# Performance work log

Measured on AMD Instinct MI355X. Metric: run time of the kernel, lower is better.

Reference implementation:

```python
import jax, jax.numpy as jnp
import numpy as np

SEQ, D, H = 4096, 1024, 16
HD = D // H
SCALE = HD ** -0.5


def setup_inputs() -> dict:
    key = jax.random.key(0)
    ks = jax.random.split(key, 8)
    s = 0.02
    return {
        "hidden_states": jax.random.normal(ks[0], (SEQ, D), dtype=jnp.float32),
        "wq": jax.random.normal(ks[1], (D, D), dtype=jnp.float32) * s,
        "bq": jax.random.normal(ks[2], (D,), dtype=jnp.float32) * s,
        "wk": jax.random.normal(ks[3], (D, D), dtype=jnp.float32) * s,
        "wv": jax.random.normal(ks[4], (D, D), dtype=jnp.float32) * s,
        "bv": jax.random.normal(ks[5], (D,), dtype=jnp.float32) * s,
        "wo": jax.random.normal(ks[6], (D, D), dtype=jnp.float32) * s,
        "bo": jax.random.normal(ks[7], (D,), dtype=jnp.float32) * s,
    }


def reference(hidden_states, wq, bq, wk, wv, bv, wo, bo):
    S = hidden_states.shape[0]
    # torch Linear: y = x @ W^T + b  (k_proj has no bias)
    q = (hidden_states @ wq.T + bq).reshape(S, H, HD).transpose(1, 0, 2)  # [H,S,hd]
    k = (hidden_states @ wk.T).reshape(S, H, HD).transpose(1, 0, 2)       # [H,S,hd]
    v = (hidden_states @ wv.T + bv).reshape(S, H, HD).transpose(1, 0, 2)  # [H,S,hd]
    scores = jnp.einsum('hqd,hkd->hqk', q, k) * SCALE                     # [H,S,S]
    # softmax computed in fp32 then cast back to query dtype
    attn = jax.nn.softmax(scores.astype(jnp.float32), axis=-1).astype(q.dtype)
    out = jnp.einsum('hqk,hkd->hqd', attn, v)                             # [H,S,hd]
    out = out.transpose(1, 0, 2).reshape(S, D)
    return out @ wo.T + bo
```

## Files before the change

kernel.cpp:

```cpp
#include <hip/hip_runtime.h>

#define SEQ 4096
#define DIM 1024
#define NH 16
#define HD 64
#define QKVSTR 3072

typedef __attribute__((ext_vector_type(8))) short bf16x8;
typedef __attribute__((ext_vector_type(4))) float f32x4;
typedef __attribute__((ext_vector_type(16))) float f32x16;
typedef __attribute__((ext_vector_type(4))) unsigned int uint4v;

__device__ __forceinline__ unsigned short f2bf(float f) {
  unsigned int b = __float_as_uint(f);
  b = b + 0x7fffu + ((b >> 16) & 1u);
  return (unsigned short)(b >> 16);
}

__device__ __forceinline__ unsigned int cvt_pk_bf16(float lo, float hi) {
  unsigned int r;
  asm("v_cvt_pk_bf16_f32 %0, %1, %2" : "=v"(r) : "v"(lo), "v"(hi));
  return r;
}

__device__ __forceinline__ float fast_exp2(float x) {
#if __has_builtin(__builtin_amdgcn_exp2f)
  return __builtin_amdgcn_exp2f(x);
#else
  float r; asm("v_exp_f32 %0, %1" : "=v"(r) : "v"(x)); return r;
#endif
}

typedef __attribute__((address_space(3))) unsigned int lds_uint;
typedef __attribute__((address_space(1))) const unsigned int global_uint;

__device__ __forceinline__ void gload_lds16(const void* g, void* l) {
  __builtin_amdgcn_global_load_lds((global_uint*)g, (lds_uint*)l, 16, 0, 0);
}

__global__ __launch_bounds__(256) void cast_all_kernel(
    const float* __restrict__ X, const float* __restrict__ wq, const float* __restrict__ wk,
    const float* __restrict__ wv, const float* __restrict__ wo,
    unsigned short* __restrict__ Xb, unsigned short* __restrict__ Wqkv,
    unsigned short* __restrict__ Wob, float qscale) {
  int i = blockIdx.x * 256 + threadIdx.x;
  const float* src;
  unsigned short* dst;
  float sc = 1.f;
  if (i < 524288) { src = X + (size_t)i * 8; dst = Xb + (size_t)i * 8; }
  else if (i < 655360) { int j = i - 524288; src = wq + (size_t)j * 8; dst = Wqkv + (size_t)j * 8; sc = qscale; }
  else if (i < 786432) { int j = i - 655360; src = wk + (size_t)j * 8; dst = Wqkv + 1048576 + (size_t)j * 8; }
  else if (i < 917504) { int j = i - 786432; src = wv + (size_t)j * 8; dst = Wqkv + 2097152 + (size_t)j * 8; }
  else { int j = i - 917504; src = wo + (size_t)j * 8; dst = Wob + (size_t)j * 8; }
  const float4* p = (const float4*)src;
  float4 x0 = p[0], x1 = p[1];
  union { unsigned short u[8]; uint4v v; } o;
  o.u[0] = f2bf(x0.x * sc); o.u[1] = f2bf(x0.y * sc);
  o.u[2] = f2bf(x0.z * sc); o.u[3] = f2bf(x0.w * sc);
  o.u[4] = f2bf(x1.x * sc); o.u[5] = f2bf(x1.y * sc);
  o.u[6] = f2bf(x1.z * sc); o.u[7] = f2bf(x1.w * sc);
  *(uint4v*)dst = o.v;
}

template<int BIASMODE, int OUT_F32>
__global__ __launch_bounds__(256) void gemm_bt_kernel(
    const unsigned short* __restrict__ A, const unsigned short* __restrict__ B,
    const float* __restrict__ b0, const float* __restrict__ b1, float qscale,
    void* __restrict__ Cout, int M, int N, int K) {
  __shared__ unsigned short As[2][128 * 32];
  __shared__ unsigned short Bs[2][128 * 32];
  int tid = threadIdx.x;
  int wave = tid >> 6, lane = tid & 63;
  int g = lane >> 4, lc = lane & 15;
  int wm = wave >> 1, wn = wave & 1;

  int gx = gridDim.x;
  int wgid = blockIdx.y * gx + blockIdx.x;
  int cpx = (gx * gridDim.y) >> 3;
  int sw = (wgid & 7) * cpx + (wgid >> 3);
  int m0 = (sw / gx) * 128, n0 = (sw % gx) * 128;

  int ch0 = wave * 64 + lane;
  int r0 = ch0 >> 2, cb0 = ch0 & 3;
  int ch1 = 256 + ch0;
  int r1 = ch1 >> 2, cb1 = ch1 & 3;
  const unsigned short* Ar0 = A + (size_t)(m0 + r0) * K + cb0 * 8;
  const unsigned short* Ar1 = A + (size_t)(m0 + r1) * K + cb1 * 8;
  const unsigned short* Br0 = B + (size_t)(n0 + r0) * K + cb0 * 8;
  const unsigned short* Br1 = B + (size_t)(n0 + r1) * K + cb1 * 8;
  unsigned short* sAlo[2] = { &As[0][(wave * 64) * 8],       &As[1][(wave * 64) * 8] };
  unsigned short* sAhi[2] = { &As[0][(256 + wave * 64) * 8], &As[1][(256 + wave * 64) * 8] };
  unsigned short* sBlo[2] = { &Bs[0][(wave * 64) * 8],       &Bs[1][(wave * 64) * 8] };
  unsigned short* sBhi[2] = { &Bs[0][(256 + wave * 64) * 8], &Bs[1][(256 + wave * 64) * 8] };

  f32x4 acc[4][4] = {};

  gload_lds16(Ar0, sAlo[0]);
  gload_lds16(Ar1, sAhi[0]);
  gload_lds16(Br0, sBlo[0]);
  gload_lds16(Br1, sBhi[0]);

  int cur = 0;
  for (int k0 = 0; k0 < K; k0 += 32) {
    {
      int kn = (k0 + 32 < K) ? (k0 + 32) : 0;
      int nb = cur ^ 1;
      gload_lds16(Ar0 + kn, sAlo[nb]);
      gload_lds16(Ar1 + kn, sAhi[nb]);
      gload_lds16(Br0 + kn, sBlo[nb]);
      gload_lds16(Br1 + kn, sBhi[nb]);
    }
    asm volatile("s_waitcnt vmcnt(4)" ::: "memory");
    __builtin_amdgcn_sched_barrier(0);
    __builtin_amdgcn_s_barrier();
    __builtin_amdgcn_sched_barrier(0);

    bf16x8 af[4], bfr[4];
    for (int mf = 0; mf < 4; ++mf)
      af[mf] = *(const bf16x8*)&As[cur][(wm * 64 + mf * 16 + lc) * 32 + g * 8];
    for (int nf = 0; nf < 4; ++nf)
      bfr[nf] = *(const bf16x8*)&Bs[cur][(wn * 64 + nf * 16 + lc) * 32 + g * 8];
    for (int mf = 0; mf < 4; ++mf)
      for (int nf = 0; nf < 4; ++nf)
        acc[mf][nf] = __builtin_amdgcn_mfma_f32_16x16x32_bf16(af[mf], bfr[nf], acc[mf][nf], 0, 0, 0);

    asm volatile("" ::: "memory");
    __builtin_amdgcn_sched_barrier(0);
    __builtin_amdgcn_s_barrier();
    cur ^= 1;
  }

  for (int nf = 0; nf < 4; ++nf) {
    int col = n0 + wn * 64 + nf * 16 + lc;
    float bias = 0.f;
    if (BIASMODE == 1) {
      int sect = col >> 10, cc = col & 1023;
      bias = (sect == 0) ? b0[cc] * qscale : ((sect == 2) ? b1[cc] : 0.f);
    } else if (BIASMODE == 2) {
      bias = b0[col];
    }
    for (int mf = 0; mf < 4; ++mf) {
      int row = m0 + wm * 64 + mf * 16 + g * 4;
      for (int r = 0; r < 4; ++r) {
        float v = acc[mf][nf][r] + bias;
        if (OUT_F32) ((float*)Cout)[(size_t)(row + r) * N + col] = v;
        else ((unsigned short*)Cout)[(size_t)(row + r) * N + col] = f2bf(v);
      }
    }
  }
}

__global__ __launch_bounds__(256) void transpose_kernel(
    const unsigned short* __restrict__ V, unsigned short* __restrict__ Vt) {
  __shared__ unsigned short Ts[64 * 72];
  int tid = threadIdx.x;
  int s0 = blockIdx.x * 64, d0 = blockIdx.y * 64;
  for (int c = 0; c < 2; ++c) {
    int q = c * 256 + tid;
    int r = q >> 3, cb = q & 7;
    uint4v v = *(const uint4v*)&V[(size_t)(s0 + r) * QKVSTR + d0 + cb * 8];
    *(uint4v*)&Ts[r * 72 + cb * 8] = v;
  }
  __syncthreads();
  for (int c = 0; c < 2; ++c) {
    int q = c * 256 + tid;
    int d = q >> 3, sc = q & 7;
    union { unsigned short u[8]; uint4v v; } ov;
    for (int j = 0; j < 8; ++j) ov.u[j] = Ts[(sc * 8 + j) * 72 + d];
    *(uint4v*)&Vt[(size_t)(d0 + d) * SEQ + s0 + sc * 8] = ov.v;
  }
}

__global__ __launch_bounds__(256) void attn_kernel(
    const unsigned short* __restrict__ QKV, const unsigned short* __restrict__ Vt,
    unsigned short* __restrict__ Aout) {
  __shared__ unsigned short Qs[128 * 64];
  __shared__ unsigned short Ks[2][64 * 64];
  __shared__ unsigned short Vs[2][64 * 64];
  int tid = threadIdx.x;
  int w = tid >> 6, lane = tid & 63;
  int hi = lane >> 5, l31 = lane & 31;

  int bid = blockIdx.x;
  int swz = (bid & 7) * 64 + (bid >> 3);
  int h = swz >> 5;
  int q0 = (swz & 31) * 128;

  const unsigned short* Qg = QKV + h * HD;
  const unsigned short* Kg = QKV + DIM + h * HD;
  const unsigned short* Vg = Vt + (size_t)(h * HD) * SEQ;

  int ch0 = w * 64 + lane;
  int r0s = ch0 >> 3, d0s = (ch0 & 7) ^ (r0s & 7);
  int ch1 = 256 + ch0;
  int r1s = ch1 >> 3, d1s = (ch1 & 7) ^ (r1s & 7);
  size_t koff0 = (size_t)r0s * QKVSTR + d0s * 8;
  size_t koff1 = (size_t)r1s * QKVSTR + d1s * 8;
  size_t voff0 = (size_t)r0s * SEQ + d0s * 8;
  size_t voff1 = (size_t)r1s * SEQ + d1s * 8;
  unsigned short* ldsK_lo[2] = { &Ks[0][(w * 64) * 8],       &Ks[1][(w * 64) * 8] };
  unsigned short* ldsK_hi[2] = { &Ks[0][(256 + w * 64) * 8], &Ks[1][(256 + w * 64) * 8] };
  unsigned short* ldsV_lo[2] = { &Vs[0][(w * 64) * 8],       &Vs[1][(w * 64) * 8] };
  unsigned short* ldsV_hi[2] = { &Vs[0][(256 + w * 64) * 8], &Vs[1][(256 + w * 64) * 8] };

  for (int c = 0; c < 4; ++c) {
    int chunk = c * 256 + w * 64 + lane;
    int row = chunk >> 3, pos = chunk & 7;
    int db = pos ^ (row & 7);
    gload_lds16(Qg + (size_t)(q0 + row) * QKVSTR + db * 8, Qs + (c * 256 + w * 64) * 8);
  }
  gload_lds16(Kg + koff0, ldsK_lo[0]);
  gload_lds16(Kg + koff1, ldsK_hi[0]);
  gload_lds16(Vg + voff0, ldsV_lo[0]);
  gload_lds16(Vg + voff1, ldsV_hi[0]);
  asm volatile("s_waitcnt vmcnt(4)" ::: "memory");
  __builtin_amdgcn_sched_barrier(0);
  __builtin_amdgcn_s_barrier();

  bf16x8 qf[4];
  {
    int qrow = w * 32 + l31;
    for (int dc = 0; dc < 4; ++dc) {
      int pos = 2 * dc + hi;
      qf[dc] = *(const bf16x8*)&Qs[qrow * 64 + (pos ^ (qrow & 7)) * 8];
    }
  }

  int offb[4];
#pragma unroll
  for (int dc = 0; dc < 4; ++dc)
    offb[dc] = l31 * 128 + (((2 * dc + hi) ^ (l31 & 7)) * 16);
  const char* KbA = (const char*)&Ks[0][0];
  const char* KbB = (const char*)&Ks[1][0];
  const char* VbA = (const char*)&Vs[0][0];
  const char* VbB = (const char*)&Vs[1][0];

  union { unsigned short us[8]; bf16x8 v; } one8;
#pragma unroll
  for (int j = 0; j < 8; ++j) one8.us[j] = 0x3F80;

  f32x16 o0 = {}, o1 = {}, lsa = {};
  int cur = 0;

  for (int t = 0; t < SEQ / 64; ++t) {
    {
      int kvn = ((t + 1) & (SEQ / 64 - 1)) * 64;
      const unsigned short* Kt = Kg + (size_t)kvn * QKVSTR;
      const unsigned short* Vtt = Vg + kvn;
      int nb = cur ^ 1;
      gload_lds16(Kt + koff0, ldsK_lo[nb]);
      gload_lds16(Kt + koff1, ldsK_hi[nb]);
      gload_lds16(Vtt + voff0, ldsV_lo[nb]);
      gload_lds16(Vtt + voff1, ldsV_hi[nb]);
    }
    asm volatile("s_waitcnt vmcnt(4)" ::: "memory");
    __builtin_amdgcn_sched_barrier(0);
    __builtin_amdgcn_s_barrier();
    __builtin_amdgcn_sched_barrier(0);

    const char* Kb = cur ? KbB : KbA;
    const char* Vb = cur ? VbB : VbA;

    bf16x8 kf0[4], kf1[4];
#pragma unroll
    for (int dc = 0; dc < 4; ++dc) {
      kf0[dc] = *(const bf16x8*)(Kb + offb[dc]);
      kf1[dc] = *(const bf16x8*)(Kb + offb[dc] + 4096);
    }
    f32x16 st0 = {}, st1 = {};
    __builtin_amdgcn_s_setprio(1);
#pragma unroll
    for (int dc = 0; dc < 4; ++dc) {
      st0 = __builtin_amdgcn_mfma_f32_32x32x16_bf16(kf0[dc], qf[dc], st0, 0, 0, 0);
      st1 = __builtin_amdgcn_mfma_f32_32x32x16_bf16(kf1[dc], qf[dc], st1, 0, 0, 0);
    }
    __builtin_amdgcn_s_setprio(0);

    bf16x8 vf0[4], vf1[4];
#pragma unroll
    for (int c = 0; c < 4; ++c) {
      vf0[c] = *(const bf16x8*)(Vb + offb[c]);
      vf1[c] = *(const bf16x8*)(Vb + offb[c] + 4096);
    }

    float p0[16], p1[16];
#pragma unroll
    for (int r = 0; r < 16; ++r) p0[r] = fast_exp2(st0[r]);
#pragma unroll
    for (int r = 0; r < 16; ++r) p1[r] = fast_exp2(st1[r]);

    bf16x8 pa[4];
#pragma unroll
    for (int f = 0; f < 2; ++f) {
      const float* pp = f ? p1 : p0;
#pragma unroll
      for (int cc = 0; cc < 2; ++cc) {
        unsigned uLO0 = cvt_pk_bf16(pp[8 * cc + 0], pp[8 * cc + 1]);
        unsigned uLO1 = cvt_pk_bf16(pp[8 * cc + 2], pp[8 * cc + 3]);
        unsigned uHI0 = cvt_pk_bf16(pp[8 * cc + 4], pp[8 * cc + 5]);
        unsigned uHI1 = cvt_pk_bf16(pp[8 * cc + 6], pp[8 * cc + 7]);
        auto s0 = __builtin_amdgcn_permlane32_swap(uLO0, uHI0, false, false);
        auto s1 = __builtin_amdgcn_permlane32_swap(uLO1, uHI1, false, false);
        union { unsigned u[4]; bf16x8 v; } pw;
        pw.u[0] = s0[0]; pw.u[1] = s1[0]; pw.u[2] = s0[1]; pw.u[3] = s1[1];
        pa[f * 2 + cc] = pw.v;
      }
    }

    __builtin_amdgcn_s_setprio(1);
#pragma unroll
    for (int c = 0; c < 4; ++c) {
      o0 = __builtin_amdgcn_mfma_f32_32x32x16_bf16(pa[c], vf0[c], o0, 0, 0, 0);
      o1 = __builtin_amdgcn_mfma_f32_32x32x16_bf16(pa[c], vf1[c], o1, 0, 0, 0);
      lsa = __builtin_amdgcn_mfma_f32_32x32x16_bf16(pa[c], one8.v, lsa, 0, 0, 0);
    }
    __builtin_amdgcn_s_setprio(0);

    asm volatile("" ::: "memory");
    __builtin_amdgcn_sched_barrier(0);
    __builtin_amdgcn_s_barrier();
    cur ^= 1;
  }

  float* Qf = (float*)Qs;
  if (l31 == 0) {
#pragma unroll
    for (int r = 0; r < 16; ++r)
      Qf[w * 32 + ((r & 3) + 8 * (r >> 2) + 4 * hi)] = lsa[r];
  }
  float inv = 1.f / Qf[w * 32 + l31];
#pragma unroll
  for (int r = 0; r < 16; ++r) {
    int qr = (r & 3) + 8 * (r >> 2) + 4 * hi;
    float ir = __shfl(inv, qr + (lane & 32));
    size_t row = q0 + w * 32 + qr;
    Aout[row * DIM + h * HD + l31]      = f2bf(o0[r] * ir);
    Aout[row * DIM + h * HD + 32 + l31] = f2bf(o1[r] * ir);
  }
}

extern "C" void kernel_launch(void* const* d_in, const int* in_sizes, int n_in,
                              void* d_out, int out_size, void* d_ws, size_t ws_size,
                              hipStream_t stream) {
  (void)in_sizes; (void)n_in; (void)out_size; (void)ws_size;
  const float* X  = (const float*)d_in[0];
  const float* wq = (const float*)d_in[1];
  const float* bq = (const float*)d_in[2];
  const float* wk = (const float*)d_in[3];
  const float* wv = (const float*)d_in[4];
  const float* bv = (const float*)d_in[5];
  const float* wo = (const float*)d_in[6];
  const float* bo = (const float*)d_in[7];

  char* ws = (char*)d_ws;
  const size_t SZ_XD  = (size_t)SEQ * DIM * 2;
  const size_t SZ_W   = (size_t)DIM * DIM * 2;
  const size_t SZ_QKV = (size_t)SEQ * QKVSTR * 2;
  unsigned short* Xb   = (unsigned short*)(ws);
  unsigned short* Wqkv = (unsigned short*)(ws + SZ_XD);
  unsigned short* Wob  = (unsigned short*)(ws + SZ_XD + 3 * SZ_W);
  unsigned short* QKVb = (unsigned short*)(ws + SZ_XD + 4 * SZ_W);
  unsigned short* Vtb  = (unsigned short*)(ws + SZ_XD + 4 * SZ_W + SZ_QKV);
  unsigned short* Ab   = Xb;

  const float QSCALE = 0.125f * 1.44269504088896f;

  cast_all_kernel<<<4096, 256, 0, stream>>>(X, wq, wk, wv, wo, Xb, Wqkv, Wob, QSCALE);

  gemm_bt_kernel<1, 0><<<dim3(QKVSTR / 128, SEQ / 128), 256, 0, stream>>>(
      Xb, Wqkv, bq, bv, QSCALE, QKVb, SEQ, QKVSTR, DIM);

  transpose_kernel<<<dim3(SEQ / 64, DIM / 64), 256, 0, stream>>>(QKVb + 2 * DIM, Vtb);

  attn_kernel<<<SEQ / 128 * NH, 256, 0, stream>>>(QKVb, Vtb, Ab);

  gemm_bt_kernel<2, 1><<<dim3(DIM / 128, SEQ / 128), 256, 0, stream>>>(
      Ab, Wob, bo, nullptr, 1.f, d_out, SEQ, DIM, DIM);
}
```

Measured before the change: 167.3 us.

## Process two 64-key tiles per barrier with 128-key double-buffered LDS stages

The attention main loop now loads 128 keys/values per stage into a doubled LDS buffer and runs the 64-key compute body twice per iteration. This halves the number of block-wide barriers and wait points, and deepens each prefetch. In exchange LDS use roughly doubles (Q plus 4x K/V tiles), which can lower occupancy, and the unrolled body doubles the code size.

```diff
diff --git a/kernel.cpp b/kernel.cpp
--- a/kernel.cpp
+++ b/kernel.cpp
@@ -175,8 +175,8 @@
     const unsigned short* __restrict__ QKV, const unsigned short* __restrict__ Vt,
     unsigned short* __restrict__ Aout) {
   __shared__ unsigned short Qs[128 * 64];
-  __shared__ unsigned short Ks[2][64 * 64];
-  __shared__ unsigned short Vs[2][64 * 64];
+  __shared__ unsigned short Ks[2][2][64 * 64];
+  __shared__ unsigned short Vs[2][2][64 * 64];
   int tid = threadIdx.x;
   int w = tid >> 6, lane = tid & 63;
   int hi = lane >> 5, l31 = lane & 31;
@@ -198,10 +198,16 @@
   size_t koff1 = (size_t)r1s * QKVSTR + d1s * 8;
   size_t voff0 = (size_t)r0s * SEQ + d0s * 8;
   size_t voff1 = (size_t)r1s * SEQ + d1s * 8;
-  unsigned short* ldsK_lo[2] = { &Ks[0][(w * 64) * 8],       &Ks[1][(w * 64) * 8] };
-  unsigned short* ldsK_hi[2] = { &Ks[0][(256 + w * 64) * 8], &Ks[1][(256 + w * 64) * 8] };
-  unsigned short* ldsV_lo[2] = { &Vs[0][(w * 64) * 8],       &Vs[1][(w * 64) * 8] };
-  unsigned short* ldsV_hi[2] = { &Vs[0][(256 + w * 64) * 8], &Vs[1][(256 + w * 64) * 8] };
+  unsigned short* ldsK_lo[2][2], *ldsK_hi[2][2], *ldsV_lo[2][2], *ldsV_hi[2][2];
+#pragma unroll
+  for (int b = 0; b < 2; ++b)
+#pragma unroll
+    for (int hh = 0; hh < 2; ++hh) {
+      ldsK_lo[b][hh] = &Ks[b][hh][(w * 64) * 8];
+      ldsK_hi[b][hh] = &Ks[b][hh][(256 + w * 64) * 8];
+      ldsV_lo[b][hh] = &Vs[b][hh][(w * 64) * 8];
+      ldsV_hi[b][hh] = &Vs[b][hh][(256 + w * 64) * 8];
+    }
 
   for (int c = 0; c < 4; ++c) {
     int chunk = c * 256 + w * 64 + lane;
@@ -209,11 +215,21 @@
     int db = pos ^ (row & 7);
     gload_lds16(Qg + (size_t)(q0 + row) * QKVSTR + db * 8, Qs + (c * 256 + w * 64) * 8);
   }
-  gload_lds16(Kg + koff0, ldsK_lo[0]);
-  gload_lds16(Kg + koff1, ldsK_hi[0]);
-  gload_lds16(Vg + voff0, ldsV_lo[0]);
-  gload_lds16(Vg + voff1, ldsV_hi[0]);
-  asm volatile("s_waitcnt vmcnt(4)" ::: "memory");
+  {
+    const unsigned short* K0 = Kg;
+    const unsigned short* K1 = Kg + (size_t)64 * QKVSTR;
+    const unsigned short* V0 = Vg;
+    const unsigned short* V1 = Vg + 64;
+    gload_lds16(K0 + koff0, ldsK_lo[0][0]);
+    gload_lds16(K0 + koff1, ldsK_hi[0][0]);
+    gload_lds16(K1 + koff0, ldsK_lo[0][1]);
+    gload_lds16(K1 + koff1, ldsK_hi[0][1]);
+    gload_lds16(V0 + voff0, ldsV_lo[0][0]);
+    gload_lds16(V0 + voff1, ldsV_hi[0][0]);
+    gload_lds16(V1 + voff0, ldsV_lo[0][1]);
+    gload_lds16(V1 + voff1, ldsV_hi[0][1]);
+  }
+  asm volatile("s_waitcnt vmcnt(8)" ::: "memory");
   __builtin_amdgcn_sched_barrier(0);
   __builtin_amdgcn_s_barrier();
 
@@ -230,37 +246,14 @@
 #pragma unroll
   for (int dc = 0; dc < 4; ++dc)
     offb[dc] = l31 * 128 + (((2 * dc + hi) ^ (l31 & 7)) * 16);
-  const char* KbA = (const char*)&Ks[0][0];
-  const char* KbB = (const char*)&Ks[1][0];
-  const char* VbA = (const char*)&Vs[0][0];
-  const char* VbB = (const char*)&Vs[1][0];
 
   union { unsigned short us[8]; bf16x8 v; } one8;
 #pragma unroll
   for (int j = 0; j < 8; ++j) one8.us[j] = 0x3F80;
 
   f32x16 o0 = {}, o1 = {}, lsa = {};
-  int cur = 0;
-
-  for (int t = 0; t < SEQ / 64; ++t) {
-    {
-      int kvn = ((t + 1) & (SEQ / 64 - 1)) * 64;
-      const unsigned short* Kt = Kg + (size_t)kvn * QKVSTR;
-      const unsigned short* Vtt = Vg + kvn;
-      int nb = cur ^ 1;
-      gload_lds16(Kt + koff0, ldsK_lo[nb]);
-      gload_lds16(Kt + koff1, ldsK_hi[nb]);
-      gload_lds16(Vtt + voff0, ldsV_lo[nb]);
-      gload_lds16(Vtt + voff1, ldsV_hi[nb]);
-    }
-    asm volatile("s_waitcnt vmcnt(4)" ::: "memory");
-    __builtin_amdgcn_sched_barrier(0);
-    __builtin_amdgcn_s_barrier();
-    __builtin_amdgcn_sched_barrier(0);
-
-    const char* Kb = cur ? KbB : KbA;
-    const char* Vb = cur ? VbB : VbA;
-
+
+  auto half_body = [&](const char* Kb, const char* Vb) {
     bf16x8 kf0[4], kf1[4];
 #pragma unroll
     for (int dc = 0; dc < 4; ++dc) {
@@ -315,6 +308,38 @@
       lsa = __builtin_amdgcn_mfma_f32_32x32x16_bf16(pa[c], one8.v, lsa, 0, 0, 0);
     }
     __builtin_amdgcn_s_setprio(0);
+  };
+
+  int cur = 0;
+  for (int t = 0; t < SEQ / 128; ++t) {
+    {
+      int kvn = ((t + 1) & (SEQ / 128 - 1)) * 128;
+      const unsigned short* K0 = Kg + (size_t)kvn * QKVSTR;
+      const unsigned short* K1 = K0 + (size_t)64 * QKVSTR;
+      const unsigned short* V0 = Vg + kvn;
+      const unsigned short* V1 = V0 + 64;
+      int nb = cur ^ 1;
+      gload_lds16(K0 + koff0, ldsK_lo[nb][0]);
+      gload_lds16(K0 + koff1, ldsK_hi[nb][0]);
+      gload_lds16(K1 + koff0, ldsK_lo[nb][1]);
+      gload_lds16(K1 + koff1, ldsK_hi[nb][1]);
+      gload_lds16(V0 + voff0, ldsV_lo[nb][0]);
+      gload_lds16(V0 + voff1, ldsV_hi[nb][0]);
+      gload_lds16(V1 + voff0, ldsV_lo[nb][1]);
+      gload_lds16(V1 + voff1, ldsV_hi[nb][1]);
+    }
+    asm volatile("s_waitcnt vmcnt(8)" ::: "memory");
+    __builtin_amdgcn_sched_barrier(0);
+    __builtin_amdgcn_s_barrier();
+    __builtin_amdgcn_sched_barrier(0);
+
+    if (cur == 0) {
+      half_body((const char*)&Ks[0][0][0], (const char*)&Vs[0][0][0]);
+      half_body((const char*)&Ks[0][1][0], (const char*)&Vs[0][1][0]);
+    } else {
+      half_body((const char*)&Ks[1][0][0], (const char*)&Vs[1][0][0]);
+      half_body((const char*)&Ks[1][1][0], (const char*)&Vs[1][1][0]);
+    }
 
     asm volatile("" ::: "memory");
     __builtin_amdgcn_sched_barrier(0);
```

New measurement: 171.9 us. 2.8% more time.
